# Kernel tuning notes

Hardware: AMD Instinct MI355X
Metric: run time of the kernel (lower is better)

## Reference

```python
import jax, jax.numpy as jnp
import numpy as np
import math

N_DRUG, N_DIS, D, EMB, HEADS, STEPS = 3072, 3072, 64, 16, 4, 5
N = N_DRUG + N_DIS


def setup_inputs() -> dict:
    key = jax.random.key(0)
    ks = jax.random.split(key, 16)
    s = lambda fan: 1.0 / np.sqrt(fan)
    return {
        "graph": jax.random.uniform(ks[0], (N, N), jnp.float32),
        "drug_f": jax.random.normal(ks[1], (N_DRUG, D), jnp.float32),
        "disease_f": jax.random.normal(ks[2], (N_DIS, D), jnp.float32),
        "timesteps": jax.random.randint(ks[3], (N,), 0, STEPS, jnp.int32),
        "drug_w": jax.random.normal(ks[4], (D, D), jnp.float32) * s(D),
        "disease_w": jax.random.normal(ks[5], (D, D), jnp.float32) * s(D),
        "emb_w": jax.random.normal(ks[6], (EMB, EMB), jnp.float32) * s(EMB),
        "emb_b": jnp.zeros((EMB,), jnp.float32),
        "in_w": jax.random.normal(ks[7], (D + EMB, 256), jnp.float32) * s(D + EMB),
        "in_b": jnp.zeros((256,), jnp.float32),
        "out_w": jax.random.normal(ks[8], (256, D), jnp.float32) * s(256),
        "out_b": jnp.zeros((D,), jnp.float32),
        "wq": jax.random.normal(ks[9], (D, D), jnp.float32) * s(D),
        "bq": jnp.zeros((D,), jnp.float32),
        "wk": jax.random.normal(ks[10], (D, D), jnp.float32) * s(D),
        "bk": jnp.zeros((D,), jnp.float32),
        "wv": jax.random.normal(ks[11], (D, D), jnp.float32) * s(D),
        "bv": jnp.zeros((D,), jnp.float32),
        "wo": jax.random.normal(ks[12], (D, D), jnp.float32) * s(D),
        "bo": jnp.zeros((D,), jnp.float32),
        "fuse_w": jax.random.normal(ks[13], (2 * D, D), jnp.float32) * s(2 * D),
        "fuse_b": jnp.zeros((D,), jnp.float32),
        "ln_g": jnp.ones((D,), jnp.float32),
        "ln_b": jnp.zeros((D,), jnp.float32),
    }


def _layernorm(x, g, b, eps=1e-5):
    mu = jnp.mean(x, axis=-1, keepdims=True)
    var = jnp.var(x, axis=-1, keepdims=True)
    return (x - mu) * jax.lax.rsqrt(var + eps) * g + b


def reference(graph, drug_f, disease_f, timesteps, drug_w, disease_w,
              emb_w, emb_b, in_w, in_b, out_w, out_b,
              wq, bq, wk, bk, wv, bv, wo, bo,
              fuse_w, fuse_b, ln_g, ln_b):
    # ---- DGLLayer: per-type projection + symmetric degree-norm propagation ----
    node_f = jnp.concatenate([drug_f @ drug_w, disease_f @ disease_w], axis=0)  # [N, D]
    degs = jnp.clip(jnp.sum(graph, axis=1), 1.0, None)
    norm = jax.lax.rsqrt(degs)[:, None]  # degs^-0.5, [N, 1]
    target = (graph @ (node_f * norm)) * norm

    # ---- Denoise MLP with sinusoidal time embedding ----
    half = EMB // 2
    freqs = jnp.exp(-math.log(10000.0) * jnp.arange(half, dtype=jnp.float32) / half)
    temp = timesteps.astype(jnp.float32)[:, None] * freqs[None]  # [N, half]
    time_emb = jnp.concatenate([jnp.cos(temp), jnp.sin(temp)], axis=-1)  # [N, EMB]
    emb = time_emb @ emb_w + emb_b
    h = jnp.concatenate([target, emb], axis=-1)  # [N, D+EMB]
    h = jnp.tanh(h @ in_w + in_b)  # in-layer
    aux = h @ out_w + out_b        # final out-layer (no tanh)

    # ---- AttentionFusion: cross-attention(target -> aux) + fuse + residual LN ----
    hd = D // HEADS
    q = (target @ wq + bq).reshape(N, HEADS, hd)
    k = (aux @ wk + bk).reshape(N, HEADS, hd)
    v = (aux @ wv + bv).reshape(N, HEADS, hd)
    scores = jnp.einsum('nhd,mhd->hnm', q, k) / np.sqrt(hd)  # [H, N, N]
    attn = jax.nn.softmax(scores, axis=-1)
    attn_out = jnp.einsum('hnm,mhd->nhd', attn, v).reshape(N, D) @ wo + bo
    fused = jnp.concatenate([target, attn_out], axis=-1) @ fuse_w + fuse_b
    return _layernorm(fused + target, ln_g, ln_b)
```

## Files before the change

### kernel.cpp

```cpp
#include <hip/hip_runtime.h>
#include <cstdint>
#include <cstddef>

#define NTOT 6144
#define NDRUG 3072
#define NM (NTOT*64)

typedef __fp16 f16;
typedef __attribute__((ext_vector_type(4))) __fp16 f16x4;
typedef __attribute__((ext_vector_type(8))) __fp16 f16x8;
typedef __attribute__((ext_vector_type(4))) float f32x4;

__global__ __launch_bounds__(256) void k_deg(const float* __restrict__ g,
                                             const float* __restrict__ drug_f,
                                             const float* __restrict__ dis_f,
                                             const float* __restrict__ drug_w,
                                             const float* __restrict__ dis_w,
                                             float* __restrict__ norm,
                                             f16* __restrict__ gh,
                                             f16* __restrict__ nfst){
  __shared__ float sx[4][64];
  __shared__ float snf[4][64];
  int wv = threadIdx.x >> 6, j = threadIdx.x & 63;
  int row = blockIdx.x*4 + wv;
  const float4* p = (const float4*)(g + (size_t)row * NTOT);
  f16* ghrow = gh + (size_t)row * NTOT;
  float s = 0.f;
  #pragma unroll
  for (int it = 0; it < 24; ++it) {
    float4 u = p[it*64 + j];
    s += (u.x + u.y) + (u.z + u.w);
    f16x4 pk = {(f16)u.x, (f16)u.y, (f16)u.z, (f16)u.w};
    *(f16x4*)(ghrow + (size_t)(it*64 + j)*4) = pk;
  }
  #pragma unroll
  for (int off = 32; off; off >>= 1) s += __shfl_xor(s, off, 64);
  float nrm = rsqrtf(fmaxf(s, 1.0f));
  if (j == 0) norm[row] = nrm;

  const float* x; const float* W;
  if (row < NDRUG){ x = drug_f + (size_t)row*64; W = drug_w; }
  else            { x = dis_f + (size_t)(row-NDRUG)*64; W = dis_w; }
  sx[wv][j] = x[j];
  __syncthreads();
  float acc = 0.f;
  #pragma unroll 8
  for (int k = 0; k < 64; ++k) acc = fmaf(sx[wv][k], W[k*64+j], acc);
  snf[wv][j] = acc * nrm;
  __syncthreads();
  if (threadIdx.x < 64){
    int c = threadIdx.x;
    f16x4 pk = {(f16)snf[0][c], (f16)snf[1][c], (f16)snf[2][c], (f16)snf[3][c]};
    *(f16x4*)(nfst + (size_t)c*NTOT + blockIdx.x*4) = pk;
  }
}

__global__ __launch_bounds__(256) void k_gemm(const f16* __restrict__ gh,
                                              const f16* __restrict__ nfst,
                                              float* __restrict__ part){
  __shared__ f16 sA[2][64][72];
  __shared__ f16 sB[2][64][72];
  const int tid = threadIdx.x;
  const int lane = tid & 63, w = tid >> 6;
  const int l15 = lane & 15, quad = lane >> 4;
  const int row0 = blockIdx.x * 64;
  const int kbase = blockIdx.y * 768;
  const int sr = tid >> 2, scg = (tid & 3) * 16;

  f32x4 acc[4] = {{0.f,0.f,0.f,0.f},{0.f,0.f,0.f,0.f},
                  {0.f,0.f,0.f,0.f},{0.f,0.f,0.f,0.f}};
  f16x8 ra0, ra1, rb0, rb1;
  auto LOADT = [&](int kt){
    const f16* pa = gh + (size_t)(row0 + sr)*NTOT + kbase + kt*64 + scg;
    ra0 = *(const f16x8*)pa; ra1 = *(const f16x8*)(pa + 8);
    const f16* pb = nfst + (size_t)sr*NTOT + kbase + kt*64 + scg;
    rb0 = *(const f16x8*)pb; rb1 = *(const f16x8*)(pb + 8);
  };
  auto WRITET = [&](int b){
    *(f16x8*)&sA[b][sr][scg]     = ra0;
    *(f16x8*)&sA[b][sr][scg + 8] = ra1;
    *(f16x8*)&sB[b][sr][scg]     = rb0;
    *(f16x8*)&sB[b][sr][scg + 8] = rb1;
  };
  LOADT(0); WRITET(0);
  int cur = 0;
  for (int kt = 0; kt < 12; ++kt){
    if (kt < 11) LOADT(kt + 1);
    __syncthreads();
    #pragma unroll
    for (int k16 = 0; k16 < 4; ++k16){
      f16x4 af = *(const f16x4*)&sA[cur][w*16 + l15][k16*16 + quad*4];
      #pragma unroll
      for (int nt = 0; nt < 4; ++nt){
        f16x4 bf = *(const f16x4*)&sB[cur][nt*16 + l15][k16*16 + quad*4];
        acc[nt] = __builtin_amdgcn_mfma_f32_16x16x16f16(af, bf, acc[nt], 0, 0, 0);
      }
    }
    if (kt < 11) WRITET(cur ^ 1);
    cur ^= 1;
  }
  float* dst = part + (size_t)blockIdx.y * NM;
  #pragma unroll
  for (int nt = 0; nt < 4; ++nt){
    #pragma unroll
    for (int r = 0; r < 4; ++r){
      int row = row0 + w*16 + quad*4 + r;
      dst[(size_t)row*64 + nt*16 + l15] = acc[nt][r];
    }
  }
}

__global__ __launch_bounds__(256) void k_node2(const float* __restrict__ part,
                                               const float* __restrict__ norm,
                                               const int* __restrict__ ts,
                                               const float* __restrict__ emb_w,
                                               const float* __restrict__ emb_b,
                                               const float* __restrict__ in_w,
                                               const float* __restrict__ in_b,
                                               const float* __restrict__ out_w,
                                               const float* __restrict__ out_b,
                                               const float* __restrict__ wq, const float* __restrict__ bq,
                                               const float* __restrict__ wk, const float* __restrict__ bk,
                                               const float* __restrict__ wvw, const float* __restrict__ bv,
                                               float* __restrict__ target,
                                               f16* __restrict__ qh, f16* __restrict__ kh,
                                               f16* __restrict__ vt){
  __shared__ float sx[4][80];
  __shared__ float sh[4][256];
  __shared__ float sa[4][64];
  __shared__ float sv[4][64];
  int wv = threadIdx.x>>6, j = threadIdx.x&63;
  int row = blockIdx.x*4 + wv;

  float t = 0.f;
  #pragma unroll
  for (int p = 0; p < 8; ++p) t += part[(size_t)p*NM + (size_t)row*64 + j];
  t *= norm[row];
  target[(size_t)row*64 + j] = t;
  sx[wv][j] = t;
  if (j < 16) {
    const float FREQ[8] = {1.0f, 0.316227766016838f, 0.1f, 0.0316227766016838f,
                           0.01f, 0.00316227766016838f, 0.001f, 0.000316227766016838f};
    float tt = (float)ts[row];
    float e = emb_b[j];
    #pragma unroll
    for (int k = 0; k < 8; ++k) {
      float a = tt * FREQ[k];
      e = fmaf(cosf(a), emb_w[k*16 + j], e);
      e = fmaf(sinf(a), emb_w[(8+k)*16 + j], e);
    }
    sx[wv][64 + j] = e;
  }
  __syncthreads();
  float a0 = in_b[4*j+0], a1 = in_b[4*j+1], a2 = in_b[4*j+2], a3 = in_b[4*j+3];
  #pragma unroll 8
  for (int k = 0; k < 80; ++k) {
    float xv = sx[wv][k];
    float4 w = *(const float4*)(in_w + k*256 + 4*j);
    a0 = fmaf(xv, w.x, a0);
    a1 = fmaf(xv, w.y, a1);
    a2 = fmaf(xv, w.z, a2);
    a3 = fmaf(xv, w.w, a3);
  }
  sh[wv][4*j+0] = tanhf(a0); sh[wv][4*j+1] = tanhf(a1);
  sh[wv][4*j+2] = tanhf(a2); sh[wv][4*j+3] = tanhf(a3);
  __syncthreads();
  float o = out_b[j];
  #pragma unroll 8
  for (int k = 0; k < 256; ++k) o = fmaf(sh[wv][k], out_w[k*64 + j], o);
  sa[wv][j] = o;
  __syncthreads();
  float q = bq[j], kk = bk[j], vv = bv[j];
  #pragma unroll 8
  for (int k = 0; k < 64; ++k) {
    float tv = sx[wv][k], av = sa[wv][k];
    q  = fmaf(tv, wq[k*64+j],  q);
    kk = fmaf(av, wk[k*64+j],  kk);
    vv = fmaf(av, wvw[k*64+j], vv);
  }
  qh[(size_t)row*64+j] = (f16)(q * 0.25f);
  kh[(size_t)row*64+j] = (f16)kk;
  sv[wv][j] = vv;
  __syncthreads();
  if (threadIdx.x < 64){
    int c = threadIdx.x;
    f16x4 pk = {(f16)sv[0][c], (f16)sv[1][c], (f16)sv[2][c], (f16)sv[3][c]};
    *(f16x4*)(vt + (size_t)c*NTOT + blockIdx.x*4) = pk;
  }
}

__global__ __launch_bounds__(256) void k_attn(const f16* __restrict__ qh,
                                              const f16* __restrict__ kh,
                                              const f16* __restrict__ vt,
                                              float* __restrict__ pattn){
  __shared__ f16 sK[2][64][72];
  __shared__ f16 sV[2][64][72];
  const int tid = threadIdx.x;
  const int h = tid >> 6;
  const int lane = tid & 63;
  const int l15 = lane & 15, quad = lane >> 4;
  const int z = blockIdx.y;
  const int q0 = blockIdx.x * 64;

  f16x4 qf[4];
  #pragma unroll
  for (int qn = 0; qn < 4; ++qn)
    qf[qn] = *(const f16x4*)(qh + (size_t)(q0 + qn*16 + l15)*64 + h*16 + quad*4);

  f32x4 accOT[4] = {{0.f,0.f,0.f,0.f},{0.f,0.f,0.f,0.f},
                    {0.f,0.f,0.f,0.f},{0.f,0.f,0.f,0.f}};
  float lsum[4] = {0.f, 0.f, 0.f, 0.f};
  const int sr = tid >> 2, scg = (tid & 3) * 16;
  const int kbase = z * 768;
  f16x8 rk0, rk1, rv0, rv1;
  auto LOADT = [&](int kt){
    const int k0 = kbase + kt*64;
    const f16* pk = kh + (size_t)(k0 + sr)*64 + scg;
    rk0 = *(const f16x8*)pk; rk1 = *(const f16x8*)(pk + 8);
    const f16* pv = vt + (size_t)sr*NTOT + k0 + scg;
    rv0 = *(const f16x8*)pv; rv1 = *(const f16x8*)(pv + 8);
  };
  auto WRITET = [&](int b){
    *(f16x8*)&sK[b][sr][scg]     = rk0;
    *(f16x8*)&sK[b][sr][scg + 8] = rk1;
    *(f16x8*)&sV[b][sr][scg]     = rv0;
    *(f16x8*)&sV[b][sr][scg + 8] = rv1;
  };
  LOADT(0); WRITET(0);
  int cur = 0;
  for (int kt = 0; kt < 12; ++kt){
    if (kt < 11) LOADT(kt + 1);
    __syncthreads();
    #pragma unroll
    for (int km = 0; km < 4; ++km){
      f16x4 kf = *(const f16x4*)&sK[cur][km*16 + l15][h*16 + quad*4];
      f16x4 vf = *(const f16x4*)&sV[cur][h*16 + l15][km*16 + quad*4];
      #pragma unroll
      for (int qn = 0; qn < 4; ++qn){
        f32x4 s = __builtin_amdgcn_mfma_f32_16x16x16f16(
            kf, qf[qn], (f32x4){0.f,0.f,0.f,0.f}, 0, 0, 0);
        float p0 = __expf(fminf(s[0], 10.f));
        float p1 = __expf(fminf(s[1], 10.f));
        float p2 = __expf(fminf(s[2], 10.f));
        float p3 = __expf(fminf(s[3], 10.f));
        lsum[qn] += (p0 + p1) + (p2 + p3);
        f16x4 pf;
        pf[0] = (f16)p0; pf[1] = (f16)p1; pf[2] = (f16)p2; pf[3] = (f16)p3;
        accOT[qn] = __builtin_amdgcn_mfma_f32_16x16x16f16(vf, pf, accOT[qn], 0, 0, 0);
      }
    }
    if (kt < 11) WRITET(cur ^ 1);
    cur ^= 1;
  }
  #pragma unroll
  for (int qn = 0; qn < 4; ++qn){
    lsum[qn] += __shfl_xor(lsum[qn], 16, 64);
    lsum[qn] += __shfl_xor(lsum[qn], 32, 64);
  }
  #pragma unroll
  for (int qn = 0; qn < 4; ++qn){
    float* rec = pattn + ((size_t)(z*4 + h)*NTOT + q0 + qn*16 + l15) * 20;
    *(float4*)(rec + quad*4) =
        make_float4(accOT[qn][0], accOT[qn][1], accOT[qn][2], accOT[qn][3]);
    if (quad == 0){ rec[17] = lsum[qn]; }
  }
}

__global__ __launch_bounds__(256) void k_out(const float* __restrict__ pattn,
                                             const float* __restrict__ target,
                                             const float* __restrict__ wo, const float* __restrict__ bo,
                                             const float* __restrict__ fuse_w, const float* __restrict__ fuse_b,
                                             const float* __restrict__ ln_g, const float* __restrict__ ln_b,
                                             float* __restrict__ out){
  __shared__ float st[4][64], sa[4][64], sao[4][64];
  int wv = threadIdx.x>>6, j = threadIdx.x&63;
  int row = blockIdx.x*4 + wv;
  int h = j >> 4, d = j & 15;
  float osum = 0.f, L = 0.f;
  #pragma unroll
  for (int z = 0; z < 8; ++z) {
    const float* rec = pattn + ((size_t)(z*4 + h)*NTOT + row)*20;
    osum += rec[d];
    L += rec[17];
  }
  sa[wv][j] = osum / L;
  st[wv][j] = target[(size_t)row*64+j];
  __syncthreads();
  float ao = bo[j];
  #pragma unroll 8
  for (int k = 0; k < 64; ++k) ao = fmaf(sa[wv][k], wo[k*64+j], ao);
  sao[wv][j] = ao;
  __syncthreads();
  float f = fuse_b[j];
  #pragma unroll 8
  for (int k = 0; k < 64; ++k) f = fmaf(st[wv][k], fuse_w[k*64+j], f);
  #pragma unroll 8
  for (int k = 0; k < 64; ++k) f = fmaf(sao[wv][k], fuse_w[(64+k)*64+j], f);
  float x = f + st[wv][j];
  float s1 = x, s2 = x*x;
  #pragma unroll
  for (int off = 32; off; off >>= 1) { s1 += __shfl_xor(s1, off, 64); s2 += __shfl_xor(s2, off, 64); }
  float mu = s1*(1.f/64.f);
  float var = s2*(1.f/64.f) - mu*mu;
  float y = (x-mu)*rsqrtf(var + 1e-5f)*ln_g[j] + ln_b[j];
  out[(size_t)row*64 + j] = y;
}

extern "C" void kernel_launch(void* const* d_in, const int* in_sizes, int n_in,
                              void* d_out, int out_size, void* d_ws, size_t ws_size,
                              hipStream_t stream) {
  const float* graph  = (const float*)d_in[0];
  const float* drug_f = (const float*)d_in[1];
  const float* dis_f  = (const float*)d_in[2];
  const int*   ts     = (const int*)d_in[3];
  const float* drug_w = (const float*)d_in[4];
  const float* dis_w  = (const float*)d_in[5];
  const float* emb_w  = (const float*)d_in[6];
  const float* emb_b  = (const float*)d_in[7];
  const float* in_w   = (const float*)d_in[8];
  const float* in_b   = (const float*)d_in[9];
  const float* out_w  = (const float*)d_in[10];
  const float* out_b  = (const float*)d_in[11];
  const float* wq     = (const float*)d_in[12];
  const float* bq     = (const float*)d_in[13];
  const float* wk     = (const float*)d_in[14];
  const float* bk     = (const float*)d_in[15];
  const float* wvw    = (const float*)d_in[16];
  const float* bv     = (const float*)d_in[17];
  const float* wo     = (const float*)d_in[18];
  const float* bo     = (const float*)d_in[19];
  const float* fuse_w = (const float*)d_in[20];
  const float* fuse_b = (const float*)d_in[21];
  const float* ln_g   = (const float*)d_in[22];
  const float* ln_b   = (const float*)d_in[23];

  float* ws     = (float*)d_ws;
  float* norm   = ws;
  f16*   gh     = (f16*)(ws + 8192);
  float* base   = ws + 8192 + (size_t)NTOT*NTOT/2;
  f16*   nfst   = (f16*)base;
  float* target = base + (size_t)64*NTOT/2;
  f16*   qh     = (f16*)(target + NM);
  f16*   kh     = (f16*)(target + NM + NM/2);
  f16*   vt     = (f16*)(target + NM + NM);
  float* part   = target + NM + NM + NM/2;
  float* pattn  = part + (size_t)8*NM;

  k_deg<<<1536, 256, 0, stream>>>(graph, drug_f, dis_f, drug_w, dis_w, norm, gh, nfst);
  k_gemm<<<dim3(96, 8), 256, 0, stream>>>(gh, nfst, part);
  k_node2<<<1536, 256, 0, stream>>>(part, norm, ts, emb_w, emb_b, in_w, in_b,
                                    out_w, out_b, wq, bq, wk, bk, wvw, bv,
                                    target, qh, kh, vt);
  k_attn<<<dim3(96, 8), 256, 0, stream>>>(qh, kh, vt, pattn);
  k_out<<<1536, 256, 0, stream>>>(pattn, target, wo, bo, fuse_w, fuse_b,
                                  ln_g, ln_b, (float*)d_out);
}
```

Before: 399.0 us.

## Fuse all five stages into one persistent kernel with grid barriers

Replaces the five separate kernel launches with a single persistent kernel of 768 blocks that runs each stage in turn, separated by atomic-counter grid barriers. The barrier counters are zeroed with a memset before the launch. Row-wise stages now process two 4-row groups per block. This removes four launch gaps and the tail effects between kernels, but adds spin-wait barrier cost. It also relies on all 768 blocks being co-resident, or the kernel deadlocks.

```diff
diff --git a/kernel.cpp b/kernel.cpp
--- a/kernel.cpp
+++ b/kernel.cpp
@@ -5,353 +5,367 @@
 #define NTOT 6144
 #define NDRUG 3072
 #define NM (NTOT*64)
+#define NBLK 768
 
 typedef __fp16 f16;
 typedef __attribute__((ext_vector_type(4))) __fp16 f16x4;
 typedef __attribute__((ext_vector_type(8))) __fp16 f16x8;
 typedef __attribute__((ext_vector_type(4))) float f32x4;
 
-__global__ __launch_bounds__(256) void k_deg(const float* __restrict__ g,
-                                             const float* __restrict__ drug_f,
-                                             const float* __restrict__ dis_f,
-                                             const float* __restrict__ drug_w,
-                                             const float* __restrict__ dis_w,
-                                             float* __restrict__ norm,
-                                             f16* __restrict__ gh,
-                                             f16* __restrict__ nfst){
-  __shared__ float sx[4][64];
-  __shared__ float snf[4][64];
-  int wv = threadIdx.x >> 6, j = threadIdx.x & 63;
-  int row = blockIdx.x*4 + wv;
-  const float4* p = (const float4*)(g + (size_t)row * NTOT);
-  f16* ghrow = gh + (size_t)row * NTOT;
-  float s = 0.f;
-  #pragma unroll
-  for (int it = 0; it < 24; ++it) {
-    float4 u = p[it*64 + j];
-    s += (u.x + u.y) + (u.z + u.w);
-    f16x4 pk = {(f16)u.x, (f16)u.y, (f16)u.z, (f16)u.w};
-    *(f16x4*)(ghrow + (size_t)(it*64 + j)*4) = pk;
-  }
-  #pragma unroll
-  for (int off = 32; off; off >>= 1) s += __shfl_xor(s, off, 64);
-  float nrm = rsqrtf(fmaxf(s, 1.0f));
-  if (j == 0) norm[row] = nrm;
-
-  const float* x; const float* W;
-  if (row < NDRUG){ x = drug_f + (size_t)row*64; W = drug_w; }
-  else            { x = dis_f + (size_t)(row-NDRUG)*64; W = dis_w; }
-  sx[wv][j] = x[j];
+struct KParams {
+  const float *graph, *drug_f, *dis_f;
+  const int   *ts;
+  const float *drug_w, *dis_w, *emb_w, *emb_b, *in_w, *in_b, *out_w, *out_b;
+  const float *wq, *bq, *wk, *bkp, *wvw, *bv, *wo, *bo, *fuse_w, *fuse_b, *ln_g, *ln_b;
+  float *norm; f16 *gh; f16 *nfst;
+  float *target; f16 *qh; f16 *kh; f16 *vt;
+  float *part; float *pattn; float *out;
+  unsigned *bar;
+};
+
+__device__ __forceinline__ void gridbar(unsigned* c){
   __syncthreads();
-  float acc = 0.f;
-  #pragma unroll 8
-  for (int k = 0; k < 64; ++k) acc = fmaf(sx[wv][k], W[k*64+j], acc);
-  snf[wv][j] = acc * nrm;
+  if (threadIdx.x == 0){
+    __threadfence();
+    __hip_atomic_fetch_add(c, 1u, __ATOMIC_ACQ_REL, __HIP_MEMORY_SCOPE_AGENT);
+    while (__hip_atomic_load(c, __ATOMIC_ACQUIRE, __HIP_MEMORY_SCOPE_AGENT) < NBLK)
+      __builtin_amdgcn_s_sleep(16);
+    __threadfence();
+  }
   __syncthreads();
-  if (threadIdx.x < 64){
-    int c = threadIdx.x;
-    f16x4 pk = {(f16)snf[0][c], (f16)snf[1][c], (f16)snf[2][c], (f16)snf[3][c]};
-    *(f16x4*)(nfst + (size_t)c*NTOT + blockIdx.x*4) = pk;
-  }
 }
 
-__global__ __launch_bounds__(256) void k_gemm(const f16* __restrict__ gh,
-                                              const f16* __restrict__ nfst,
-                                              float* __restrict__ part){
-  __shared__ f16 sA[2][64][72];
-  __shared__ f16 sB[2][64][72];
+__global__ __launch_bounds__(256, 3) void k_all(KParams P){
+  __shared__ __align__(16) char smem[36864];
   const int tid = threadIdx.x;
-  const int lane = tid & 63, w = tid >> 6;
-  const int l15 = lane & 15, quad = lane >> 4;
-  const int row0 = blockIdx.x * 64;
-  const int kbase = blockIdx.y * 768;
-  const int sr = tid >> 2, scg = (tid & 3) * 16;
-
-  f32x4 acc[4] = {{0.f,0.f,0.f,0.f},{0.f,0.f,0.f,0.f},
-                  {0.f,0.f,0.f,0.f},{0.f,0.f,0.f,0.f}};
-  f16x8 ra0, ra1, rb0, rb1;
-  auto LOADT = [&](int kt){
-    const f16* pa = gh + (size_t)(row0 + sr)*NTOT + kbase + kt*64 + scg;
-    ra0 = *(const f16x8*)pa; ra1 = *(const f16x8*)(pa + 8);
-    const f16* pb = nfst + (size_t)sr*NTOT + kbase + kt*64 + scg;
-    rb0 = *(const f16x8*)pb; rb1 = *(const f16x8*)(pb + 8);
-  };
-  auto WRITET = [&](int b){
-    *(f16x8*)&sA[b][sr][scg]     = ra0;
-    *(f16x8*)&sA[b][sr][scg + 8] = ra1;
-    *(f16x8*)&sB[b][sr][scg]     = rb0;
-    *(f16x8*)&sB[b][sr][scg + 8] = rb1;
-  };
-  LOADT(0); WRITET(0);
-  int cur = 0;
-  for (int kt = 0; kt < 12; ++kt){
-    if (kt < 11) LOADT(kt + 1);
-    __syncthreads();
+  const int wv = tid >> 6, j = tid & 63;
+  const int bx = blockIdx.x;
+
+  {
+    float (*sx)[64]  = (float(*)[64])smem;
+    float (*snf)[64] = (float(*)[64])(smem + 1024);
+    for (int half = 0; half < 2; ++half){
+      const int bi = bx*2 + half;
+      const int row = bi*4 + wv;
+      const float4* p = (const float4*)(P.graph + (size_t)row * NTOT);
+      f16* ghrow = P.gh + (size_t)row * NTOT;
+      float s = 0.f;
+      #pragma unroll
+      for (int it = 0; it < 24; ++it) {
+        float4 u = p[it*64 + j];
+        s += (u.x + u.y) + (u.z + u.w);
+        f16x4 pk = {(f16)u.x, (f16)u.y, (f16)u.z, (f16)u.w};
+        *(f16x4*)(ghrow + (size_t)(it*64 + j)*4) = pk;
+      }
+      #pragma unroll
+      for (int off = 32; off; off >>= 1) s += __shfl_xor(s, off, 64);
+      float nrm = rsqrtf(fmaxf(s, 1.0f));
+      if (j == 0) P.norm[row] = nrm;
+
+      const float* x; const float* W;
+      if (row < NDRUG){ x = P.drug_f + (size_t)row*64; W = P.drug_w; }
+      else            { x = P.dis_f + (size_t)(row-NDRUG)*64; W = P.dis_w; }
+      sx[wv][j] = x[j];
+      __syncthreads();
+      float acc = 0.f;
+      #pragma unroll 8
+      for (int k = 0; k < 64; ++k) acc = fmaf(sx[wv][k], W[k*64+j], acc);
+      snf[wv][j] = acc * nrm;
+      __syncthreads();
+      if (tid < 64){
+        int c = tid;
+        f16x4 pk = {(f16)snf[0][c], (f16)snf[1][c], (f16)snf[2][c], (f16)snf[3][c]};
+        *(f16x4*)(P.nfst + (size_t)c*NTOT + bi*4) = pk;
+      }
+      __syncthreads();
+    }
+  }
+  gridbar(P.bar + 0);
+
+  {
+    typedef f16 (*TileP)[64][72];
+    TileP sA = (TileP)smem;
+    TileP sB = (TileP)(smem + 18432);
+    const int lane = tid & 63, w = tid >> 6;
+    const int l15 = lane & 15, quad = lane >> 4;
+    const int xb = bx % 96, z = bx / 96;
+    const int row0 = xb * 64;
+    const int kbase = z * 768;
+    const int sr = tid >> 2, scg = (tid & 3) * 16;
+
+    f32x4 acc[4] = {{0.f,0.f,0.f,0.f},{0.f,0.f,0.f,0.f},
+                    {0.f,0.f,0.f,0.f},{0.f,0.f,0.f,0.f}};
+    f16x8 ra0, ra1, rb0, rb1;
+    auto LOADT = [&](int kt){
+      const f16* pa = P.gh + (size_t)(row0 + sr)*NTOT + kbase + kt*64 + scg;
+      ra0 = *(const f16x8*)pa; ra1 = *(const f16x8*)(pa + 8);
+      const f16* pb = P.nfst + (size_t)sr*NTOT + kbase + kt*64 + scg;
+      rb0 = *(const f16x8*)pb; rb1 = *(const f16x8*)(pb + 8);
+    };
+    auto WRITET = [&](int b){
+      *(f16x8*)&sA[b][sr][scg]     = ra0;
+      *(f16x8*)&sA[b][sr][scg + 8] = ra1;
+      *(f16x8*)&sB[b][sr][scg]     = rb0;
+      *(f16x8*)&sB[b][sr][scg + 8] = rb1;
+    };
+    LOADT(0); WRITET(0);
+    int cur = 0;
+    for (int kt = 0; kt < 12; ++kt){
+      if (kt < 11) LOADT(kt + 1);
+      __syncthreads();
+      #pragma unroll
+      for (int k16 = 0; k16 < 4; ++k16){
+        f16x4 af = *(const f16x4*)&sA[cur][w*16 + l15][k16*16 + quad*4];
+        #pragma unroll
+        for (int nt = 0; nt < 4; ++nt){
+          f16x4 bf = *(const f16x4*)&sB[cur][nt*16 + l15][k16*16 + quad*4];
+          acc[nt] = __builtin_amdgcn_mfma_f32_16x16x16f16(af, bf, acc[nt], 0, 0, 0);
+        }
+      }
+      if (kt < 11) WRITET(cur ^ 1);
+      cur ^= 1;
+      if (kt < 11) __syncthreads();
+    }
+    float* dst = P.part + (size_t)z * NM;
     #pragma unroll
-    for (int k16 = 0; k16 < 4; ++k16){
-      f16x4 af = *(const f16x4*)&sA[cur][w*16 + l15][k16*16 + quad*4];
-      #pragma unroll
-      for (int nt = 0; nt < 4; ++nt){
-        f16x4 bf = *(const f16x4*)&sB[cur][nt*16 + l15][k16*16 + quad*4];
-        acc[nt] = __builtin_amdgcn_mfma_f32_16x16x16f16(af, bf, acc[nt], 0, 0, 0);
-      }
-    }
-    if (kt < 11) WRITET(cur ^ 1);
-    cur ^= 1;
-  }
-  float* dst = part + (size_t)blockIdx.y * NM;
-  #pragma unroll
-  for (int nt = 0; nt < 4; ++nt){
+    for (int nt = 0; nt < 4; ++nt){
+      #pragma unroll
+      for (int r = 0; r < 4; ++r){
+        int row = row0 + w*16 + quad*4 + r;
+        dst[(size_t)row*64 + nt*16 + l15] = acc[nt][r];
+      }
+    }
+  }
+  gridbar(P.bar + 1);
+
+  {
+    float (*sx)[80]  = (float(*)[80])smem;
+    float (*sh)[256] = (float(*)[256])(smem + 1280);
+    float (*sa)[64]  = (float(*)[64])(smem + 5376);
+    float (*sv)[64]  = (float(*)[64])(smem + 6400);
+    for (int half = 0; half < 2; ++half){
+      const int bi = bx*2 + half;
+      const int row = bi*4 + wv;
+      float t = 0.f;
+      #pragma unroll
+      for (int p = 0; p < 8; ++p) t += P.part[(size_t)p*NM + (size_t)row*64 + j];
+      t *= P.norm[row];
+      P.target[(size_t)row*64 + j] = t;
+      sx[wv][j] = t;
+      if (j < 16) {
+        const float FREQ[8] = {1.0f, 0.316227766016838f, 0.1f, 0.0316227766016838f,
+                               0.01f, 0.00316227766016838f, 0.001f, 0.000316227766016838f};
+        float tt = (float)P.ts[row];
+        float e = P.emb_b[j];
+        #pragma unroll
+        for (int k = 0; k < 8; ++k) {
+          float a = tt * FREQ[k];
+          e = fmaf(cosf(a), P.emb_w[k*16 + j], e);
+          e = fmaf(sinf(a), P.emb_w[(8+k)*16 + j], e);
+        }
+        sx[wv][64 + j] = e;
+      }
+      __syncthreads();
+      float a0 = P.in_b[4*j+0], a1 = P.in_b[4*j+1], a2 = P.in_b[4*j+2], a3 = P.in_b[4*j+3];
+      #pragma unroll 8
+      for (int k = 0; k < 80; ++k) {
+        float xv = sx[wv][k];
+        float4 w = *(const float4*)(P.in_w + k*256 + 4*j);
+        a0 = fmaf(xv, w.x, a0);
+        a1 = fmaf(xv, w.y, a1);
+        a2 = fmaf(xv, w.z, a2);
+        a3 = fmaf(xv, w.w, a3);
+      }
+      sh[wv][4*j+0] = tanhf(a0); sh[wv][4*j+1] = tanhf(a1);
+      sh[wv][4*j+2] = tanhf(a2); sh[wv][4*j+3] = tanhf(a3);
+      __syncthreads();
+      float o = P.out_b[j];
+      #pragma unroll 8
+      for (int k = 0; k < 256; ++k) o = fmaf(sh[wv][k], P.out_w[k*64 + j], o);
+      sa[wv][j] = o;
+      __syncthreads();
+      float q = P.bq[j], kk = P.bkp[j], vvv = P.bv[j];
+      #pragma unroll 8
+      for (int k = 0; k < 64; ++k) {
+        float tv = sx[wv][k], av = sa[wv][k];
+        q   = fmaf(tv, P.wq[k*64+j],  q);
+        kk  = fmaf(av, P.wk[k*64+j],  kk);
+        vvv = fmaf(av, P.wvw[k*64+j], vvv);
+      }
+      P.qh[(size_t)row*64+j] = (f16)(q * 0.25f);
+      P.kh[(size_t)row*64+j] = (f16)kk;
+      sv[wv][j] = vvv;
+      __syncthreads();
+      if (tid < 64){
+        int c = tid;
+        f16x4 pk = {(f16)sv[0][c], (f16)sv[1][c], (f16)sv[2][c], (f16)sv[3][c]};
+        *(f16x4*)(P.vt + (size_t)c*NTOT + bi*4) = pk;
+      }
+      __syncthreads();
+    }
+  }
+  gridbar(P.bar + 2);
+
+  {
+    typedef f16 (*TileP)[64][72];
+    TileP sK = (TileP)smem;
+    TileP sV = (TileP)(smem + 18432);
+    const int h = tid >> 6;
+    const int lane = tid & 63;
+    const int l15 = lane & 15, quad = lane >> 4;
+    const int z = bx / 96;
+    const int q0 = (bx % 96) * 64;
+
+    f16x4 qf[4];
     #pragma unroll
-    for (int r = 0; r < 4; ++r){
-      int row = row0 + w*16 + quad*4 + r;
-      dst[(size_t)row*64 + nt*16 + l15] = acc[nt][r];
-    }
-  }
-}
-
-__global__ __launch_bounds__(256) void k_node2(const float* __restrict__ part,
-                                               const float* __restrict__ norm,
-                                               const int* __restrict__ ts,
-                                               const float* __restrict__ emb_w,
-                                               const float* __restrict__ emb_b,
-                                               const float* __restrict__ in_w,
-                                               const float* __restrict__ in_b,
-                                               const float* __restrict__ out_w,
-                                               const float* __restrict__ out_b,
-                                               const float* __restrict__ wq, const float* __restrict__ bq,
-                                               const float* __restrict__ wk, const float* __restrict__ bk,
-                                               const float* __restrict__ wvw, const float* __restrict__ bv,
-                                               float* __restrict__ target,
-                                               f16* __restrict__ qh, f16* __restrict__ kh,
-                                               f16* __restrict__ vt){
-  __shared__ float sx[4][80];
-  __shared__ float sh[4][256];
-  __shared__ float sa[4][64];
-  __shared__ float sv[4][64];
-  int wv = threadIdx.x>>6, j = threadIdx.x&63;
-  int row = blockIdx.x*4 + wv;
-
-  float t = 0.f;
-  #pragma unroll
-  for (int p = 0; p < 8; ++p) t += part[(size_t)p*NM + (size_t)row*64 + j];
-  t *= norm[row];
-  target[(size_t)row*64 + j] = t;
-  sx[wv][j] = t;
-  if (j < 16) {
-    const float FREQ[8] = {1.0f, 0.316227766016838f, 0.1f, 0.0316227766016838f,
-                           0.01f, 0.00316227766016838f, 0.001f, 0.000316227766016838f};
-    float tt = (float)ts[row];
-    float e = emb_b[j];
+    for (int qn = 0; qn < 4; ++qn)
+      qf[qn] = *(const f16x4*)(P.qh + (size_t)(q0 + qn*16 + l15)*64 + h*16 + quad*4);
+
+    f32x4 accOT[4] = {{0.f,0.f,0.f,0.f},{0.f,0.f,0.f,0.f},
+                      {0.f,0.f,0.f,0.f},{0.f,0.f,0.f,0.f}};
+    float lsum[4] = {0.f, 0.f, 0.f, 0.f};
+    const int sr = tid >> 2, scg = (tid & 3) * 16;
+    const int kbase = z * 768;
+    f16x8 rk0, rk1, rv0, rv1;
+    auto LOADT = [&](int kt){
+      const int k0 = kbase + kt*64;
+      const f16* pk = P.kh + (size_t)(k0 + sr)*64 + scg;
+      rk0 = *(const f16x8*)pk; rk1 = *(const f16x8*)(pk + 8);
+      const f16* pv = P.vt + (size_t)sr*NTOT + k0 + scg;
+      rv0 = *(const f16x8*)pv; rv1 = *(const f16x8*)(pv + 8);
+    };
+    auto WRITET = [&](int b){
+      *(f16x8*)&sK[b][sr][scg]     = rk0;
+      *(f16x8*)&sK[b][sr][scg + 8] = rk1;
+      *(f16x8*)&sV[b][sr][scg]     = rv0;
+      *(f16x8*)&sV[b][sr][scg + 8] = rv1;
+    };
+    LOADT(0); WRITET(0);
+    int cur = 0;
+    for (int kt = 0; kt < 12; ++kt){
+      if (kt < 11) LOADT(kt + 1);
+      __syncthreads();
+      #pragma unroll
+      for (int km = 0; km < 4; ++km){
+        f16x4 kf = *(const f16x4*)&sK[cur][km*16 + l15][h*16 + quad*4];
+        f16x4 vf = *(const f16x4*)&sV[cur][h*16 + l15][km*16 + quad*4];
+        #pragma unroll
+        for (int qn = 0; qn < 4; ++qn){
+          f32x4 s = __builtin_amdgcn_mfma_f32_16x16x16f16(
+              kf, qf[qn], (f32x4){0.f,0.f,0.f,0.f}, 0, 0, 0);
+          float p0 = __expf(fminf(s[0], 10.f));
+          float p1 = __expf(fminf(s[1], 10.f));
+          float p2 = __expf(fminf(s[2], 10.f));
+          float p3 = __expf(fminf(s[3], 10.f));
+          lsum[qn] += (p0 + p1) + (p2 + p3);
+          f16x4 pf;
+          pf[0] = (f16)p0; pf[1] = (f16)p1; pf[2] = (f16)p2; pf[3] = (f16)p3;
+          accOT[qn] = __builtin_amdgcn_mfma_f32_16x16x16f16(vf, pf, accOT[qn], 0, 0, 0);
+        }
+      }
+      if (kt < 11) WRITET(cur ^ 1);
+      cur ^= 1;
+      if (kt < 11) __syncthreads();
+    }
     #pragma unroll
-    for (int k = 0; k < 8; ++k) {
-      float a = tt * FREQ[k];
-      e = fmaf(cosf(a), emb_w[k*16 + j], e);
-      e = fmaf(sinf(a), emb_w[(8+k)*16 + j], e);
-    }
-    sx[wv][64 + j] = e;
-  }
-  __syncthreads();
-  float a0 = in_b[4*j+0], a1 = in_b[4*j+1], a2 = in_b[4*j+2], a3 = in_b[4*j+3];
-  #pragma unroll 8
-  for (int k = 0; k < 80; ++k) {
-    float xv = sx[wv][k];
-    float4 w = *(const float4*)(in_w + k*256 + 4*j);
-    a0 = fmaf(xv, w.x, a0);
-    a1 = fmaf(xv, w.y, a1);
-    a2 = fmaf(xv, w.z, a2);
-    a3 = fmaf(xv, w.w, a3);
-  }
-  sh[wv][4*j+0] = tanhf(a0); sh[wv][4*j+1] = tanhf(a1);
-  sh[wv][4*j+2] = tanhf(a2); sh[wv][4*j+3] = tanhf(a3);
-  __syncthreads();
-  float o = out_b[j];
-  #pragma unroll 8
-  for (int k = 0; k < 256; ++k) o = fmaf(sh[wv][k], out_w[k*64 + j], o);
-  sa[wv][j] = o;
-  __syncthreads();
-  float q = bq[j], kk = bk[j], vv = bv[j];
-  #pragma unroll 8
-  for (int k = 0; k < 64; ++k) {
-    float tv = sx[wv][k], av = sa[wv][k];
-    q  = fmaf(tv, wq[k*64+j],  q);
-    kk = fmaf(av, wk[k*64+j],  kk);
-    vv = fmaf(av, wvw[k*64+j], vv);
-  }
-  qh[(size_t)row*64+j] = (f16)(q * 0.25f);
-  kh[(size_t)row*64+j] = (f16)kk;
-  sv[wv][j] = vv;
-  __syncthreads();
-  if (threadIdx.x < 64){
-    int c = threadIdx.x;
-    f16x4 pk = {(f16)sv[0][c], (f16)sv[1][c], (f16)sv[2][c], (f16)sv[3][c]};
-    *(f16x4*)(vt + (size_t)c*NTOT + blockIdx.x*4) = pk;
-  }
-}
-
-__global__ __launch_bounds__(256) void k_attn(const f16* __restrict__ qh,
-                                              const f16* __restrict__ kh,
-                                              const f16* __restrict__ vt,
-                                              float* __restrict__ pattn){
-  __shared__ f16 sK[2][64][72];
-  __shared__ f16 sV[2][64][72];
-  const int tid = threadIdx.x;
-  const int h = tid >> 6;
-  const int lane = tid & 63;
-  const int l15 = lane & 15, quad = lane >> 4;
-  const int z = blockIdx.y;
-  const int q0 = blockIdx.x * 64;
-
-  f16x4 qf[4];
-  #pragma unroll
-  for (int qn = 0; qn < 4; ++qn)
-    qf[qn] = *(const f16x4*)(qh + (size_t)(q0 + qn*16 + l15)*64 + h*16 + quad*4);
-
-  f32x4 accOT[4] = {{0.f,0.f,0.f,0.f},{0.f,0.f,0.f,0.f},
-                    {0.f,0.f,0.f,0.f},{0.f,0.f,0.f,0.f}};
-  float lsum[4] = {0.f, 0.f, 0.f, 0.f};
-  const int sr = tid >> 2, scg = (tid & 3) * 16;
-  const int kbase = z * 768;
-  f16x8 rk0, rk1, rv0, rv1;
-  auto LOADT = [&](int kt){
-    const int k0 = kbase + kt*64;
-    const f16* pk = kh + (size_t)(k0 + sr)*64 + scg;
-    rk0 = *(const f16x8*)pk; rk1 = *(const f16x8*)(pk + 8);
-    const f16* pv = vt + (size_t)sr*NTOT + k0 + scg;
-    rv0 = *(const f16x8*)pv; rv1 = *(const f16x8*)(pv + 8);
-  };
-  auto WRITET = [&](int b){
-    *(f16x8*)&sK[b][sr][scg]     = rk0;
-    *(f16x8*)&sK[b][sr][scg + 8] = rk1;
-    *(f16x8*)&sV[b][sr][scg]     = rv0;
-    *(f16x8*)&sV[b][sr][scg + 8] = rv1;
-  };
-  LOADT(0); WRITET(0);
-  int cur = 0;
-  for (int kt = 0; kt < 12; ++kt){
-    if (kt < 11) LOADT(kt + 1);
-    __syncthreads();
+    for (int qn = 0; qn < 4; ++qn){
+      lsum[qn] += __shfl_xor(lsum[qn], 16, 64);
+      lsum[qn] += __shfl_xor(lsum[qn], 32, 64);
+    }
     #pragma unroll
-    for (int km = 0; km < 4; ++km){
-      f16x4 kf = *(const f16x4*)&sK[cur][km*16 + l15][h*16 + quad*4];
-      f16x4 vf = *(const f16x4*)&sV[cur][h*16 + l15][km*16 + quad*4];
-      #pragma unroll
-      for (int qn = 0; qn < 4; ++qn){
-        f32x4 s = __builtin_amdgcn_mfma_f32_16x16x16f16(
-            kf, qf[qn], (f32x4){0.f,0.f,0.f,0.f}, 0, 0, 0);
-        float p0 = __expf(fminf(s[0], 10.f));
-        float p1 = __expf(fminf(s[1], 10.f));
-        float p2 = __expf(fminf(s[2], 10.f));
-        float p3 = __expf(fminf(s[3], 10.f));
-        lsum[qn] += (p0 + p1) + (p2 + p3);
-        f16x4 pf;
-        pf[0] = (f16)p0; pf[1] = (f16)p1; pf[2] = (f16)p2; pf[3] = (f16)p3;
-        accOT[qn] = __builtin_amdgcn_mfma_f32_16x16x16f16(vf, pf, accOT[qn], 0, 0, 0);
-      }
-    }
-    if (kt < 11) WRITET(cur ^ 1);
-    cur ^= 1;
-  }
-  #pragma unroll
-  for (int qn = 0; qn < 4; ++qn){
-    lsum[qn] += __shfl_xor(lsum[qn], 16, 64);
-    lsum[qn] += __shfl_xor(lsum[qn], 32, 64);
-  }
-  #pragma unroll
-  for (int qn = 0; qn < 4; ++qn){
-    float* rec = pattn + ((size_t)(z*4 + h)*NTOT + q0 + qn*16 + l15) * 20;
-    *(float4*)(rec + quad*4) =
-        make_float4(accOT[qn][0], accOT[qn][1], accOT[qn][2], accOT[qn][3]);
-    if (quad == 0){ rec[17] = lsum[qn]; }
-  }
-}
-
-__global__ __launch_bounds__(256) void k_out(const float* __restrict__ pattn,
-                                             const float* __restrict__ target,
-                                             const float* __restrict__ wo, const float* __restrict__ bo,
-                                             const float* __restrict__ fuse_w, const float* __restrict__ fuse_b,
-                                             const float* __restrict__ ln_g, const float* __restrict__ ln_b,
-                                             float* __restrict__ out){
-  __shared__ float st[4][64], sa[4][64], sao[4][64];
-  int wv = threadIdx.x>>6, j = threadIdx.x&63;
-  int row = blockIdx.x*4 + wv;
-  int h = j >> 4, d = j & 15;
-  float osum = 0.f, L = 0.f;
-  #pragma unroll
-  for (int z = 0; z < 8; ++z) {
-    const float* rec = pattn + ((size_t)(z*4 + h)*NTOT + row)*20;
-    osum += rec[d];
-    L += rec[17];
-  }
-  sa[wv][j] = osum / L;
-  st[wv][j] = target[(size_t)row*64+j];
-  __syncthreads();
-  float ao = bo[j];
-  #pragma unroll 8
-  for (int k = 0; k < 64; ++k) ao = fmaf(sa[wv][k], wo[k*64+j], ao);
-  sao[wv][j] = ao;
-  __syncthreads();
-  float f = fuse_b[j];
-  #pragma unroll 8
-  for (int k = 0; k < 64; ++k) f = fmaf(st[wv][k], fuse_w[k*64+j], f);
-  #pragma unroll 8
-  for (int k = 0; k < 64; ++k) f = fmaf(sao[wv][k], fuse_w[(64+k)*64+j], f);
-  float x = f + st[wv][j];
-  float s1 = x, s2 = x*x;
-  #pragma unroll
-  for (int off = 32; off; off >>= 1) { s1 += __shfl_xor(s1, off, 64); s2 += __shfl_xor(s2, off, 64); }
-  float mu = s1*(1.f/64.f);
-  float var = s2*(1.f/64.f) - mu*mu;
-  float y = (x-mu)*rsqrtf(var + 1e-5f)*ln_g[j] + ln_b[j];
-  out[(size_t)row*64 + j] = y;
+    for (int qn = 0; qn < 4; ++qn){
+      float* rec = P.pattn + ((size_t)(z*4 + h)*NTOT + q0 + qn*16 + l15) * 20;
+      *(float4*)(rec + quad*4) =
+          make_float4(accOT[qn][0], accOT[qn][1], accOT[qn][2], accOT[qn][3]);
+      if (quad == 0){ rec[17] = lsum[qn]; }
+    }
+  }
+  gridbar(P.bar + 3);
+
+  {
+    float (*st)[64]  = (float(*)[64])smem;
+    float (*sa)[64]  = (float(*)[64])(smem + 1024);
+    float (*sao)[64] = (float(*)[64])(smem + 2048);
+    const int h = j >> 4, d = j & 15;
+    for (int half = 0; half < 2; ++half){
+      const int bi = bx*2 + half;
+      const int row = bi*4 + wv;
+      float osum = 0.f, L = 0.f;
+      #pragma unroll
+      for (int z = 0; z < 8; ++z) {
+        const float* rec = P.pattn + ((size_t)(z*4 + h)*NTOT + row)*20;
+        osum += rec[d];
+        L += rec[17];
+      }
+      sa[wv][j] = osum / L;
+      st[wv][j] = P.target[(size_t)row*64+j];
+      __syncthreads();
+      float ao = P.bo[j];
+      #pragma unroll 8
+      for (int k = 0; k < 64; ++k) ao = fmaf(sa[wv][k], P.wo[k*64+j], ao);
+      sao[wv][j] = ao;
+      __syncthreads();
+      float f = P.fuse_b[j];
+      #pragma unroll 8
+      for (int k = 0; k < 64; ++k) f = fmaf(st[wv][k], P.fuse_w[k*64+j], f);
+      #pragma unroll 8
+      for (int k = 0; k < 64; ++k) f = fmaf(sao[wv][k], P.fuse_w[(64+k)*64+j], f);
+      float x = f + st[wv][j];
+      float s1 = x, s2 = x*x;
+      #pragma unroll
+      for (int off = 32; off; off >>= 1) { s1 += __shfl_xor(s1, off, 64); s2 += __shfl_xor(s2, off, 64); }
+      float mu = s1*(1.f/64.f);
+      float var = s2*(1.f/64.f) - mu*mu;
+      float y = (x-mu)*rsqrtf(var + 1e-5f)*P.ln_g[j] + P.ln_b[j];
+      P.out[(size_t)row*64 + j] = y;
+      __syncthreads();
+    }
+  }
 }
 
 extern "C" void kernel_launch(void* const* d_in, const int* in_sizes, int n_in,
                               void* d_out, int out_size, void* d_ws, size_t ws_size,
                               hipStream_t stream) {
-  const float* graph  = (const float*)d_in[0];
-  const float* drug_f = (const float*)d_in[1];
-  const float* dis_f  = (const float*)d_in[2];
-  const int*   ts     = (const int*)d_in[3];
-  const float* drug_w = (const float*)d_in[4];
-  const float* dis_w  = (const float*)d_in[5];
-  const float* emb_w  = (const float*)d_in[6];
-  const float* emb_b  = (const float*)d_in[7];
-  const float* in_w   = (const float*)d_in[8];
-  const float* in_b   = (const float*)d_in[9];
-  const float* out_w  = (const float*)d_in[10];
-  const float* out_b  = (const float*)d_in[11];
-  const float* wq     = (const float*)d_in[12];
-  const float* bq     = (const float*)d_in[13];
-  const float* wk     = (const float*)d_in[14];
-  const float* bk     = (const float*)d_in[15];
-  const float* wvw    = (const float*)d_in[16];
-  const float* bv     = (const float*)d_in[17];
-  const float* wo     = (const float*)d_in[18];
-  const float* bo     = (const float*)d_in[19];
-  const float* fuse_w = (const float*)d_in[20];
-  const float* fuse_b = (const float*)d_in[21];
-  const float* ln_g   = (const float*)d_in[22];
-  const float* ln_b   = (const float*)d_in[23];
-
-  float* ws     = (float*)d_ws;
-  float* norm   = ws;
-  f16*   gh     = (f16*)(ws + 8192);
-  float* base   = ws + 8192 + (size_t)NTOT*NTOT/2;
-  f16*   nfst   = (f16*)base;
-  float* target = base + (size_t)64*NTOT/2;
-  f16*   qh     = (f16*)(target + NM);
-  f16*   kh     = (f16*)(target + NM + NM/2);
-  f16*   vt     = (f16*)(target + NM + NM);
-  float* part   = target + NM + NM + NM/2;
-  float* pattn  = part + (size_t)8*NM;
-
-  k_deg<<<1536, 256, 0, stream>>>(graph, drug_f, dis_f, drug_w, dis_w, norm, gh, nfst);
-  k_gemm<<<dim3(96, 8), 256, 0, stream>>>(gh, nfst, part);
-  k_node2<<<1536, 256, 0, stream>>>(part, norm, ts, emb_w, emb_b, in_w, in_b,
-                                    out_w, out_b, wq, bq, wk, bk, wvw, bv,
-                                    target, qh, kh, vt);
-  k_attn<<<dim3(96, 8), 256, 0, stream>>>(qh, kh, vt, pattn);
-  k_out<<<1536, 256, 0, stream>>>(pattn, target, wo, bo, fuse_w, fuse_b,
-                                  ln_g, ln_b, (float*)d_out);
+  KParams P;
+  P.graph  = (const float*)d_in[0];
+  P.drug_f = (const float*)d_in[1];
+  P.dis_f  = (const float*)d_in[2];
+  P.ts     = (const int*)d_in[3];
+  P.drug_w = (const float*)d_in[4];
+  P.dis_w  = (const float*)d_in[5];
+  P.emb_w  = (const float*)d_in[6];
+  P.emb_b  = (const float*)d_in[7];
+  P.in_w   = (const float*)d_in[8];
+  P.in_b   = (const float*)d_in[9];
+  P.out_w  = (const float*)d_in[10];
+  P.out_b  = (const float*)d_in[11];
+  P.wq     = (const float*)d_in[12];
+  P.bq     = (const float*)d_in[13];
+  P.wk     = (const float*)d_in[14];
+  P.bkp    = (const float*)d_in[15];
+  P.wvw    = (const float*)d_in[16];
+  P.bv     = (const float*)d_in[17];
+  P.wo     = (const float*)d_in[18];
+  P.bo     = (const float*)d_in[19];
+  P.fuse_w = (const float*)d_in[20];
+  P.fuse_b = (const float*)d_in[21];
+  P.ln_g   = (const float*)d_in[22];
+  P.ln_b   = (const float*)d_in[23];
+
+  float* ws = (float*)d_ws;
+  P.norm   = ws;
+  P.bar    = (unsigned*)(ws + 6656);
+  P.gh     = (f16*)(ws + 8192);
+  float* base = ws + 8192 + (size_t)NTOT*NTOT/2;
+  P.nfst   = (f16*)base;
+  P.target = base + (size_t)64*NTOT/2;
+  P.qh     = (f16*)(P.target + NM);
+  P.kh     = (f16*)(P.target + NM + NM/2);
+  P.vt     = (f16*)(P.target + NM + NM);
+  P.part   = P.target + NM + NM + NM/2;
+  P.pattn  = P.part + (size_t)8*NM;
+  P.out    = (float*)d_out;
+
+  hipMemsetAsync((void*)P.bar, 0, 64, stream);
+  k_all<<<dim3(NBLK), dim3(256), 0, stream>>>(P);
 }
```

New measurement: 1.012 ms. 154% more time.

## Read fp32 graph directly in GEMM, fold log2e into q, repack attention partials

Applied to the files above, without the earlier changes.

Removes the fp16 staging copy of the adjacency matrix: k_deg now only computes degrees, and k_gemm loads fp32 graph tiles and converts them to fp16 in registers with packed conversions. The attention softmax uses exp2 with log2(e) folded into the query scale, and uses packed fp16 conversion. Attention partials are written in a row-major layout with separate sum buffers for more coalesced writes and reads in k_out. The trade-off is that the GEMM now reads twice the bytes for the A operand, in exchange for skipping a 72MB write and a re-read.

```diff
diff --git a/kernel.cpp b/kernel.cpp
--- a/kernel.cpp
+++ b/kernel.cpp
@@ -7,9 +7,20 @@
 #define NM (NTOT*64)
 
 typedef __fp16 f16;
+typedef __attribute__((ext_vector_type(2))) __fp16 f16x2;
 typedef __attribute__((ext_vector_type(4))) __fp16 f16x4;
 typedef __attribute__((ext_vector_type(8))) __fp16 f16x8;
 typedef __attribute__((ext_vector_type(4))) float f32x4;
+
+__device__ __forceinline__ f16x8 pack8(float4 a, float4 b){
+  f16x2 p0 = __builtin_amdgcn_cvt_pkrtz(a.x, a.y);
+  f16x2 p1 = __builtin_amdgcn_cvt_pkrtz(a.z, a.w);
+  f16x2 p2 = __builtin_amdgcn_cvt_pkrtz(b.x, b.y);
+  f16x2 p3 = __builtin_amdgcn_cvt_pkrtz(b.z, b.w);
+  f16x4 lo = __builtin_shufflevector(p0, p1, 0, 1, 2, 3);
+  f16x4 hi = __builtin_shufflevector(p2, p3, 0, 1, 2, 3);
+  return __builtin_shufflevector(lo, hi, 0, 1, 2, 3, 4, 5, 6, 7);
+}
 
 __global__ __launch_bounds__(256) void k_deg(const float* __restrict__ g,
                                              const float* __restrict__ drug_f,
@@ -17,21 +28,17 @@
                                              const float* __restrict__ drug_w,
                                              const float* __restrict__ dis_w,
                                              float* __restrict__ norm,
-                                             f16* __restrict__ gh,
                                              f16* __restrict__ nfst){
   __shared__ float sx[4][64];
   __shared__ float snf[4][64];
   int wv = threadIdx.x >> 6, j = threadIdx.x & 63;
   int row = blockIdx.x*4 + wv;
   const float4* p = (const float4*)(g + (size_t)row * NTOT);
-  f16* ghrow = gh + (size_t)row * NTOT;
   float s = 0.f;
   #pragma unroll
   for (int it = 0; it < 24; ++it) {
     float4 u = p[it*64 + j];
     s += (u.x + u.y) + (u.z + u.w);
-    f16x4 pk = {(f16)u.x, (f16)u.y, (f16)u.z, (f16)u.w};
-    *(f16x4*)(ghrow + (size_t)(it*64 + j)*4) = pk;
   }
   #pragma unroll
   for (int off = 32; off; off >>= 1) s += __shfl_xor(s, off, 64);
@@ -55,7 +62,7 @@
   }
 }
 
-__global__ __launch_bounds__(256) void k_gemm(const f16* __restrict__ gh,
+__global__ __launch_bounds__(256) void k_gemm(const float* __restrict__ graph,
                                               const f16* __restrict__ nfst,
                                               float* __restrict__ part){
   __shared__ f16 sA[2][64][72];
@@ -69,16 +76,17 @@
 
   f32x4 acc[4] = {{0.f,0.f,0.f,0.f},{0.f,0.f,0.f,0.f},
                   {0.f,0.f,0.f,0.f},{0.f,0.f,0.f,0.f}};
-  f16x8 ra0, ra1, rb0, rb1;
+  float4 a0, a1, a2, a3;
+  f16x8 rb0, rb1;
   auto LOADT = [&](int kt){
-    const f16* pa = gh + (size_t)(row0 + sr)*NTOT + kbase + kt*64 + scg;
-    ra0 = *(const f16x8*)pa; ra1 = *(const f16x8*)(pa + 8);
+    const float4* pa = (const float4*)(graph + (size_t)(row0 + sr)*NTOT + kbase + kt*64 + scg);
+    a0 = pa[0]; a1 = pa[1]; a2 = pa[2]; a3 = pa[3];
     const f16* pb = nfst + (size_t)sr*NTOT + kbase + kt*64 + scg;
     rb0 = *(const f16x8*)pb; rb1 = *(const f16x8*)(pb + 8);
   };
   auto WRITET = [&](int b){
-    *(f16x8*)&sA[b][sr][scg]     = ra0;
-    *(f16x8*)&sA[b][sr][scg + 8] = ra1;
+    *(f16x8*)&sA[b][sr][scg]     = pack8(a0, a1);
+    *(f16x8*)&sA[b][sr][scg + 8] = pack8(a2, a3);
     *(f16x8*)&sB[b][sr][scg]     = rb0;
     *(f16x8*)&sB[b][sr][scg + 8] = rb1;
   };
@@ -178,7 +186,7 @@
     kk = fmaf(av, wk[k*64+j],  kk);
     vv = fmaf(av, wvw[k*64+j], vv);
   }
-  qh[(size_t)row*64+j] = (f16)(q * 0.25f);
+  qh[(size_t)row*64+j] = (f16)(q * 0.360673760222241f);
   kh[(size_t)row*64+j] = (f16)kk;
   sv[wv][j] = vv;
   __syncthreads();
@@ -192,7 +200,8 @@
 __global__ __launch_bounds__(256) void k_attn(const f16* __restrict__ qh,
                                               const f16* __restrict__ kh,
                                               const f16* __restrict__ vt,
-                                              float* __restrict__ pattn){
+                                              float* __restrict__ opart,
+                                              float* __restrict__ lpart){
   __shared__ f16 sK[2][64][72];
   __shared__ f16 sV[2][64][72];
   const int tid = threadIdx.x;
@@ -239,13 +248,14 @@
       for (int qn = 0; qn < 4; ++qn){
         f32x4 s = __builtin_amdgcn_mfma_f32_16x16x16f16(
             kf, qf[qn], (f32x4){0.f,0.f,0.f,0.f}, 0, 0, 0);
-        float p0 = __expf(fminf(s[0], 10.f));
-        float p1 = __expf(fminf(s[1], 10.f));
-        float p2 = __expf(fminf(s[2], 10.f));
-        float p3 = __expf(fminf(s[3], 10.f));
+        float p0 = exp2f(fminf(s[0], 14.4269504088896f));
+        float p1 = exp2f(fminf(s[1], 14.4269504088896f));
+        float p2 = exp2f(fminf(s[2], 14.4269504088896f));
+        float p3 = exp2f(fminf(s[3], 14.4269504088896f));
         lsum[qn] += (p0 + p1) + (p2 + p3);
-        f16x4 pf;
-        pf[0] = (f16)p0; pf[1] = (f16)p1; pf[2] = (f16)p2; pf[3] = (f16)p3;
+        f16x2 plo = __builtin_amdgcn_cvt_pkrtz(p0, p1);
+        f16x2 phi = __builtin_amdgcn_cvt_pkrtz(p2, p3);
+        f16x4 pf = __builtin_shufflevector(plo, phi, 0, 1, 2, 3);
         accOT[qn] = __builtin_amdgcn_mfma_f32_16x16x16f16(vf, pf, accOT[qn], 0, 0, 0);
       }
     }
@@ -259,14 +269,15 @@
   }
   #pragma unroll
   for (int qn = 0; qn < 4; ++qn){
-    float* rec = pattn + ((size_t)(z*4 + h)*NTOT + q0 + qn*16 + l15) * 20;
-    *(float4*)(rec + quad*4) =
+    const int row = q0 + qn*16 + l15;
+    *(float4*)(opart + (size_t)z*NM + (size_t)row*64 + h*16 + quad*4) =
         make_float4(accOT[qn][0], accOT[qn][1], accOT[qn][2], accOT[qn][3]);
-    if (quad == 0){ rec[17] = lsum[qn]; }
-  }
-}
-
-__global__ __launch_bounds__(256) void k_out(const float* __restrict__ pattn,
+    if (quad == 0) lpart[((size_t)z*4 + h)*NTOT + row] = lsum[qn];
+  }
+}
+
+__global__ __launch_bounds__(256) void k_out(const float* __restrict__ opart,
+                                             const float* __restrict__ lpart,
                                              const float* __restrict__ target,
                                              const float* __restrict__ wo, const float* __restrict__ bo,
                                              const float* __restrict__ fuse_w, const float* __restrict__ fuse_b,
@@ -275,13 +286,12 @@
   __shared__ float st[4][64], sa[4][64], sao[4][64];
   int wv = threadIdx.x>>6, j = threadIdx.x&63;
   int row = blockIdx.x*4 + wv;
-  int h = j >> 4, d = j & 15;
+  int h = j >> 4;
   float osum = 0.f, L = 0.f;
   #pragma unroll
   for (int z = 0; z < 8; ++z) {
-    const float* rec = pattn + ((size_t)(z*4 + h)*NTOT + row)*20;
-    osum += rec[d];
-    L += rec[17];
+    osum += opart[(size_t)z*NM + (size_t)row*64 + j];
+    L    += lpart[((size_t)z*4 + h)*NTOT + row];
   }
   sa[wv][j] = osum / L;
   st[wv][j] = target[(size_t)row*64+j];
@@ -336,22 +346,21 @@
 
   float* ws     = (float*)d_ws;
   float* norm   = ws;
-  f16*   gh     = (f16*)(ws + 8192);
-  float* base   = ws + 8192 + (size_t)NTOT*NTOT/2;
-  f16*   nfst   = (f16*)base;
-  float* target = base + (size_t)64*NTOT/2;
+  f16*   nfst   = (f16*)(ws + 8192);
+  float* target = ws + 8192 + (size_t)64*NTOT/2;
   f16*   qh     = (f16*)(target + NM);
   f16*   kh     = (f16*)(target + NM + NM/2);
   f16*   vt     = (f16*)(target + NM + NM);
   float* part   = target + NM + NM + NM/2;
-  float* pattn  = part + (size_t)8*NM;
-
-  k_deg<<<1536, 256, 0, stream>>>(graph, drug_f, dis_f, drug_w, dis_w, norm, gh, nfst);
-  k_gemm<<<dim3(96, 8), 256, 0, stream>>>(gh, nfst, part);
+  float* opart  = part + (size_t)8*NM;
+  float* lpart  = opart + (size_t)8*NM;
+
+  k_deg<<<1536, 256, 0, stream>>>(graph, drug_f, dis_f, drug_w, dis_w, norm, nfst);
+  k_gemm<<<dim3(96, 8), 256, 0, stream>>>(graph, nfst, part);
   k_node2<<<1536, 256, 0, stream>>>(part, norm, ts, emb_w, emb_b, in_w, in_b,
                                     out_w, out_b, wq, bq, wk, bk, wvw, bv,
                                     target, qh, kh, vt);
-  k_attn<<<dim3(96, 8), 256, 0, stream>>>(qh, kh, vt, pattn);
-  k_out<<<1536, 256, 0, stream>>>(pattn, target, wo, bo, fuse_w, fuse_b,
+  k_attn<<<dim3(96, 8), 256, 0, stream>>>(qh, kh, vt, opart, lpart);
+  k_out<<<1536, 256, 0, stream>>>(opart, lpart, target, wo, bo, fuse_w, fuse_b,
                                   ln_g, ln_b, (float*)d_out);
 }
```

Result: no change. 400.7 us (+0.4%).
